# Kernel tuning notes

Measured on AMD Instinct MI355X. Metric: run time of the kernel, lower is better.

Reference implementation:

```python
import jax, jax.numpy as jnp
import numpy as np

B, S, D, H = 64, 512, 256, 512

def setup_inputs() -> dict:
    key = jax.random.key(0)
    ks = jax.random.split(key, 16)
    s_in = 1.0 / np.sqrt(D)
    s_h = 1.0 / np.sqrt(H)
    inp = {
        "inputs": jax.random.normal(ks[0], (B, S, D), jnp.float32),
        # input-side gate weights (stored [D,H], equiv to torch Linear weight.T)
        "Wf": jax.random.uniform(ks[1], (D, H), jnp.float32, -s_in, s_in),
        "Wi": jax.random.uniform(ks[2], (D, H), jnp.float32, -s_in, s_in),
        "Wo": jax.random.uniform(ks[3], (D, H), jnp.float32, -s_in, s_in),
        "Wc": jax.random.uniform(ks[4], (D, H), jnp.float32, -s_in, s_in),
        "bf": jax.random.uniform(ks[5], (H,), jnp.float32, -s_in, s_in),
        "bi": jax.random.uniform(ks[6], (H,), jnp.float32, -s_in, s_in),
        "bo": jax.random.uniform(ks[7], (H,), jnp.float32, -s_in, s_in),
        "bc": jax.random.uniform(ks[8], (H,), jnp.float32, -s_in, s_in),
        # recurrent weights (bias=False)
        "Uf": jax.random.uniform(ks[9], (H, H), jnp.float32, -s_h, s_h),
        "Ui": jax.random.uniform(ks[10], (H, H), jnp.float32, -s_h, s_h),
        "Uo": jax.random.uniform(ks[11], (H, H), jnp.float32, -s_h, s_h),
        "Uc": jax.random.uniform(ks[12], (H, H), jnp.float32, -s_h, s_h),
        # output head
        "Wfc": jax.random.uniform(ks[13], (H, 1), jnp.float32, -s_h, s_h),
        "bfc": jax.random.uniform(ks[14], (1,), jnp.float32, -s_h, s_h),
    }
    return inp


def reference(inputs, Wf, Wi, Wo, Wc, bf, bi, bo, bc, Uf, Ui, Uo, Uc, Wfc, bfc):
    # Precompute all input-side gate projections in one big GEMM: [B,S,4H]
    Wx = jnp.concatenate([Wf, Wi, Wo, Wc], axis=1)            # [D,4H]
    bx = jnp.concatenate([bf, bi, bo, bc], axis=0)            # [4H]
    gx = jnp.einsum('bsd,dg->bsg', inputs, Wx) + bx           # [B,S,4H]
    Uh = jnp.concatenate([Uf, Ui, Uo, Uc], axis=1)            # [H,4H]

    h0 = jnp.zeros((inputs.shape[0], Uf.shape[0]), inputs.dtype)
    c0 = jnp.zeros_like(h0)
    Hd = Uf.shape[0]

    def step(carry, gx_t):
        h, c = carry
        g = gx_t + h @ Uh                                     # [B,4H]
        f_t = jax.nn.sigmoid(g[:, 0 * Hd:1 * Hd])
        i_t = jax.nn.sigmoid(g[:, 1 * Hd:2 * Hd])
        o_t = jax.nn.sigmoid(g[:, 2 * Hd:3 * Hd])
        chat = jnp.tanh(g[:, 3 * Hd:4 * Hd])
        c = f_t * c + i_t * chat
        h = o_t * jnp.tanh(c)
        return (h, c), h

    (h_t, c_t), hs = jax.lax.scan(step, (h0, c0), jnp.swapaxes(gx, 0, 1))
    outputs = jnp.swapaxes(hs, 0, 1)                          # [B,S,H]
    predictions = jnp.einsum('bsh,ho->bso', outputs, Wfc) + bfc
    return predictions, h_t, c_t
```

## Files before the change

### kernel.cpp

```cpp
#include <hip/hip_runtime.h>
#include <hip/hip_bf16.h>

#define B_ 64
#define S_ 512
#define D_ 256
#define H_ 512

typedef __attribute__((ext_vector_type(8))) short bf16x8;
typedef __attribute__((ext_vector_type(4))) float f32x4;
typedef __attribute__((ext_vector_type(4))) unsigned int uint4v;
typedef unsigned short ushort_t;
typedef unsigned long long u64_t;

__device__ __forceinline__ ushort_t f2bf(float f) {
    __hip_bfloat16 h = __float2bfloat16(f);
    return *reinterpret_cast<ushort_t*>(&h);
}
__device__ __forceinline__ float sigmoid_f(float x) { return 1.f / (1.f + __expf(-x)); }
__device__ __forceinline__ float tanh_f(float x) { return 1.f - 2.f / (__expf(2.f * x) + 1.f); }

__device__ __forceinline__ void lds_barrier() {
    asm volatile("s_waitcnt lgkmcnt(0)\n\ts_barrier" ::: "memory");
}

__global__ __launch_bounds__(512) void lstm_rec(
    const float* __restrict__ X,
    const float* __restrict__ Wf, const float* __restrict__ Wi,
    const float* __restrict__ Wo, const float* __restrict__ Wc,
    const float* __restrict__ bfp, const float* __restrict__ bip,
    const float* __restrict__ bop, const float* __restrict__ bcp,
    const float* __restrict__ Uf, const float* __restrict__ Ui,
    const float* __restrict__ Uo, const float* __restrict__ Uc,
    const float* __restrict__ Wfc,
    float* __restrict__ pred, u64_t* __restrict__ hbuf,
    unsigned int* __restrict__ xcdtab,
    float* __restrict__ outH, float* __restrict__ outC)
{
    __shared__ ushort_t hS[16 * 520];
    __shared__ ushort_t xS[16 * 264];
    __shared__ float gact[4][16][68];
    __shared__ float predS[16][512];
    __shared__ int meta[2];

    const int tid  = threadIdx.x;
    const int w    = tid >> 6;
    const int lane = tid & 63;
    const int q    = lane >> 4;
    const int m    = lane & 15;
    const int gate = w >> 1;
    const int half = w & 1;

    if (w == 0) {
        unsigned int xcd;
        asm volatile("s_getreg_b32 %0, hwreg(HW_REG_XCC_ID)" : "=s"(xcd));
        xcd &= 15u;
        if (lane == 0)
            __hip_atomic_store(&xcdtab[blockIdx.x], xcd + 1u,
                               __ATOMIC_RELEASE, __HIP_MEMORY_SCOPE_AGENT);
        unsigned int entry;
        for (;;) {
            entry = __hip_atomic_load(&xcdtab[lane], __ATOMIC_ACQUIRE, __HIP_MEMORY_SCOPE_AGENT);
            if (__ballot(entry != 0u) == ~0ull) break;
            __builtin_amdgcn_s_sleep(1);
        }
        const unsigned int xcd_j = entry - 1u;
        const unsigned int key_j = (xcd_j << 8) | (unsigned int)lane;
        const unsigned int mykey = (xcd << 8) | (unsigned int)blockIdx.x;
        const int rank = __popcll(__ballot(key_j < mykey));
        const int c_lt = __popcll(__ballot(xcd_j < xcd));
        const int c_eq = __popcll(__ballot(xcd_j == xcd));
        const int gg   = rank >> 3;
        const bool uni = (c_lt <= gg * 8) && (gg * 8 + 8 <= c_lt + c_eq);
        if (lane == 0) { meta[0] = rank; meta[1] = uni ? 1 : 0; }
    }
    __syncthreads();
    const int  rank    = meta[0];
    const bool uniform = meta[1] != 0;
    if (rank >= 32) return;
    const int g = rank >> 3;
    const int s = rank & 7;

    const int ncol0 = s * 64 + half * 32 + m;
    const int ncol1 = ncol0 + 16;

    const float* Ug = (gate == 0) ? Uf : (gate == 1) ? Ui : (gate == 2) ? Uo : Uc;
    const float* Wg = (gate == 0) ? Wf : (gate == 1) ? Wi : (gate == 2) ? Wo : Wc;
    const float* bg = (gate == 0) ? bfp : (gate == 1) ? bip : (gate == 2) ? bop : bcp;

    const float bias0 = bg[ncol0];
    const float bias1 = bg[ncol1];

    bf16x8 UF[2][16];
    bf16x8 WF[2][8];
    #pragma unroll
    for (int tt = 0; tt < 2; ++tt) {
        const int nc = tt ? ncol1 : ncol0;
        #pragma unroll
        for (int ks = 0; ks < 16; ++ks) {
            bf16x8 v;
            #pragma unroll
            for (int j = 0; j < 8; ++j)
                v[j] = (short)f2bf(Ug[(ks * 32 + q * 8 + j) * H_ + nc]);
            UF[tt][ks] = v;
        }
        #pragma unroll
        for (int ks = 0; ks < 8; ++ks) {
            bf16x8 v;
            #pragma unroll
            for (int j = 0; j < 8; ++j)
                v[j] = (short)f2bf(Wg[(ks * 32 + q * 8 + j) * H_ + nc]);
            WF[tt][ks] = v;
        }
    }

    const int urow  = tid >> 5;
    const int upair = tid & 31;
    const float2 wfc2 = *(const float2*)&Wfc[s * 64 + 2 * upair];

    float cr0 = 0.f, cr1 = 0.f;

    #pragma unroll
    for (int i = 0; i < 16; ++i)
        predS[(tid * 16 + i) >> 9][(tid * 16 + i) & 511] = 0.f;
    {
        const float* xsrc = &X[((size_t)(g * 16 + urow) * S_ + 0) * D_ + upair * 8];
        float4 a = *(const float4*)xsrc;
        float4 b = *(const float4*)(xsrc + 4);
        bf16x8 v;
        v[0] = (short)f2bf(a.x); v[1] = (short)f2bf(a.y);
        v[2] = (short)f2bf(a.z); v[3] = (short)f2bf(a.w);
        v[4] = (short)f2bf(b.x); v[5] = (short)f2bf(b.y);
        v[6] = (short)f2bf(b.z); v[7] = (short)f2bf(b.w);
        *(bf16x8*)&xS[urow * 264 + upair * 8] = v;
    }

    float4 xr0, xr1;

    for (int t = 0; t < S_; ++t) {
        {
            const int row = tid >> 5;
            const int pr  = (tid & 31) * 8;
            u64_t* pe = hbuf + ((size_t)((t & 1) * B_ + g * 16 + row) * 256 + pr);
            const unsigned int tg = (unsigned int)t;
            uint4v ra, rb;
            bool got = false;
            if (uniform) {
                uint4v r0, r1, r2, r3;
                asm volatile(
                    "global_load_dwordx4 %0, %4, off sc0\n\t"
                    "global_load_dwordx4 %1, %5, off sc0\n\t"
                    "global_load_dwordx4 %2, %6, off sc0\n\t"
                    "global_load_dwordx4 %3, %7, off sc0\n\t"
                    "s_waitcnt vmcnt(0)"
                    : "=v"(r0), "=v"(r1), "=v"(r2), "=v"(r3)
                    : "v"(pe), "v"(pe + 2), "v"(pe + 4), "v"(pe + 6)
                    : "memory");
                bool ok = r0[1] == tg && r0[3] == tg && r1[1] == tg && r1[3] == tg
                       && r2[1] == tg && r2[3] == tg && r3[1] == tg && r3[3] == tg;
                if (__ballot(ok) == ~0ull) {
                    ra[0] = r0[0]; ra[1] = r0[2]; ra[2] = r1[0]; ra[3] = r1[2];
                    rb[0] = r2[0]; rb[1] = r2[2]; rb[2] = r3[0]; rb[3] = r3[2];
                    got = true;
                }
            }
            if (!got) {
                int rounds = 0;
                for (;;) {
                    u64_t e0 = __hip_atomic_load(pe + 0, __ATOMIC_RELAXED, __HIP_MEMORY_SCOPE_AGENT);
                    u64_t e1 = __hip_atomic_load(pe + 1, __ATOMIC_RELAXED, __HIP_MEMORY_SCOPE_AGENT);
                    u64_t e2 = __hip_atomic_load(pe + 2, __ATOMIC_RELAXED, __HIP_MEMORY_SCOPE_AGENT);
                    u64_t e3 = __hip_atomic_load(pe + 3, __ATOMIC_RELAXED, __HIP_MEMORY_SCOPE_AGENT);
                    u64_t e4 = __hip_atomic_load(pe + 4, __ATOMIC_RELAXED, __HIP_MEMORY_SCOPE_AGENT);
                    u64_t e5 = __hip_atomic_load(pe + 5, __ATOMIC_RELAXED, __HIP_MEMORY_SCOPE_AGENT);
                    u64_t e6 = __hip_atomic_load(pe + 6, __ATOMIC_RELAXED, __HIP_MEMORY_SCOPE_AGENT);
                    u64_t e7 = __hip_atomic_load(pe + 7, __ATOMIC_RELAXED, __HIP_MEMORY_SCOPE_AGENT);
                    bool ok = (unsigned int)(e0 >> 32) == tg && (unsigned int)(e1 >> 32) == tg
                           && (unsigned int)(e2 >> 32) == tg && (unsigned int)(e3 >> 32) == tg
                           && (unsigned int)(e4 >> 32) == tg && (unsigned int)(e5 >> 32) == tg
                           && (unsigned int)(e6 >> 32) == tg && (unsigned int)(e7 >> 32) == tg;
                    if (__ballot(ok) == ~0ull) {
                        ra[0] = (unsigned int)e0; ra[1] = (unsigned int)e1;
                        ra[2] = (unsigned int)e2; ra[3] = (unsigned int)e3;
                        rb[0] = (unsigned int)e4; rb[1] = (unsigned int)e5;
                        rb[2] = (unsigned int)e6; rb[3] = (unsigned int)e7;
                        break;
                    }
                    if (++rounds > 2) __builtin_amdgcn_s_sleep(1);
                }
            }
            if (t + 1 < S_) {
                const float* xsrc = &X[((size_t)(g * 16 + urow) * S_ + (t + 1)) * D_ + upair * 8];
                xr0 = *(const float4*)xsrc;
                xr1 = *(const float4*)(xsrc + 4);
            }
            *(uint4v*)&hS[row * 520 + pr * 2]     = ra;
            *(uint4v*)&hS[row * 520 + pr * 2 + 8] = rb;
        }
        lds_barrier();

        f32x4 accA0 = {bias0, bias0, bias0, bias0};
        f32x4 accA1 = {bias1, bias1, bias1, bias1};
        f32x4 accB0 = {0.f, 0.f, 0.f, 0.f};
        f32x4 accB1 = {0.f, 0.f, 0.f, 0.f};
        #pragma unroll
        for (int ks = 0; ks < 8; ++ks) {
            bf16x8 a = *(const bf16x8*)&xS[m * 264 + ks * 32 + q * 8];
            accA0 = __builtin_amdgcn_mfma_f32_16x16x32_bf16(a, WF[0][ks], accA0, 0, 0, 0);
            accA1 = __builtin_amdgcn_mfma_f32_16x16x32_bf16(a, WF[1][ks], accA1, 0, 0, 0);
        }
        #pragma unroll
        for (int ks = 0; ks < 16; ++ks) {
            bf16x8 a = *(const bf16x8*)&hS[m * 520 + ks * 32 + q * 8];
            accB0 = __builtin_amdgcn_mfma_f32_16x16x32_bf16(a, UF[0][ks], accB0, 0, 0, 0);
            accB1 = __builtin_amdgcn_mfma_f32_16x16x32_bf16(a, UF[1][ks], accB1, 0, 0, 0);
        }
        #pragma unroll
        for (int j = 0; j < 4; ++j) {
            float v0 = accA0[j] + accB0[j];
            float v1 = accA1[j] + accB1[j];
            v0 = (gate < 3) ? sigmoid_f(v0) : tanh_f(v0);
            v1 = (gate < 3) ? sigmoid_f(v1) : tanh_f(v1);
            gact[gate][q * 4 + j][half * 32 + m]      = v0;
            gact[gate][q * 4 + j][half * 32 + 16 + m] = v1;
        }
        lds_barrier();

        float2 f2v = *(const float2*)&gact[0][urow][2 * upair];
        float2 i2v = *(const float2*)&gact[1][urow][2 * upair];
        float2 o2v = *(const float2*)&gact[2][urow][2 * upair];
        float2 ch2 = *(const float2*)&gact[3][urow][2 * upair];
        cr0 = f2v.x * cr0 + i2v.x * ch2.x;
        cr1 = f2v.y * cr1 + i2v.y * ch2.y;
        float hv0 = o2v.x * tanh_f(cr0);
        float hv1 = o2v.y * tanh_f(cr1);

        if (t < S_ - 1) {
            unsigned int packed = (unsigned int)f2bf(hv0) | ((unsigned int)f2bf(hv1) << 16);
            u64_t ent = ((u64_t)(unsigned int)(t + 1) << 32) | (u64_t)packed;
            u64_t* hdst = hbuf + ((size_t)(((t + 1) & 1) * B_ + g * 16 + urow) * 256
                                  + s * 32 + upair);
            asm volatile("global_store_dwordx2 %0, %1, off sc0 sc1"
                         :: "v"(hdst), "v"(ent) : "memory");
            bf16x8 v;
            v[0] = (short)f2bf(xr0.x); v[1] = (short)f2bf(xr0.y);
            v[2] = (short)f2bf(xr0.z); v[3] = (short)f2bf(xr0.w);
            v[4] = (short)f2bf(xr1.x); v[5] = (short)f2bf(xr1.y);
            v[6] = (short)f2bf(xr1.z); v[7] = (short)f2bf(xr1.w);
            *(bf16x8*)&xS[urow * 264 + upair * 8] = v;
        } else {
            *(float2*)&outH[(g * 16 + urow) * H_ + s * 64 + 2 * upair] = make_float2(hv0, hv1);
            *(float2*)&outC[(g * 16 + urow) * H_ + s * 64 + 2 * upair] = make_float2(cr0, cr1);
        }

        float pv = hv0 * wfc2.x + hv1 * wfc2.y;
        pv += __shfl_xor(pv, 16);
        pv += __shfl_xor(pv, 8);
        pv += __shfl_xor(pv, 4);
        pv += __shfl_xor(pv, 2);
        pv += __shfl_xor(pv, 1);
        if (upair == 0) predS[urow][t] = pv;
    }

    lds_barrier();
    #pragma unroll
    for (int i = 0; i < 16; ++i) {
        const int idx = tid * 16 + i;
        const int row = idx >> 9;
        const int tt  = idx & 511;
        atomicAdd(&pred[(g * 16 + row) * S_ + tt], predS[row][tt]);
    }
}

__global__ void pred_fin(const float* __restrict__ pred,
                         const float* __restrict__ bfc,
                         float* __restrict__ out)
{
    int i = blockIdx.x * blockDim.x + threadIdx.x;
    if (i < B_ * S_) out[i] = pred[i] + bfc[0];
}

extern "C" void kernel_launch(void* const* d_in, const int* in_sizes, int n_in,
                              void* d_out, int out_size, void* d_ws, size_t ws_size,
                              hipStream_t stream) {
    const float* X   = (const float*)d_in[0];
    const float* Wf  = (const float*)d_in[1];
    const float* Wi  = (const float*)d_in[2];
    const float* Wo  = (const float*)d_in[3];
    const float* Wc  = (const float*)d_in[4];
    const float* bfp = (const float*)d_in[5];
    const float* bip = (const float*)d_in[6];
    const float* bop = (const float*)d_in[7];
    const float* bcp = (const float*)d_in[8];
    const float* Uf  = (const float*)d_in[9];
    const float* Ui  = (const float*)d_in[10];
    const float* Uo  = (const float*)d_in[11];
    const float* Uc  = (const float*)d_in[12];
    const float* Wfc = (const float*)d_in[13];
    const float* bfc = (const float*)d_in[14];

    float*        pred   = (float*)d_ws;
    u64_t*        hbuf   = (u64_t*)((char*)d_ws + 131072);
    unsigned int* xcdtab = (unsigned int*)((char*)d_ws + 393216);

    hipMemsetAsync(d_ws, 0, 393216 + 256, stream);

    float* out = (float*)d_out;
    lstm_rec<<<64, 512, 0, stream>>>(X, Wf, Wi, Wo, Wc, bfp, bip, bop, bcp,
                                     Uf, Ui, Uo, Uc, Wfc,
                                     pred, hbuf, xcdtab,
                                     out + 32768, out + 65536);
    pred_fin<<<128, 256, 0, stream>>>(pred, bfc, out);
}
```

Before: 2.286 ms.

## Split waves into consumer and producer roles for cross-block h exchange

Threads are divided so the first 256 poll and load the shared hidden-state buffer and the x prefetch, each handling twice as much, while the other 256 publish h. The publishing threads stage the block's h in LDS, then write it as wider dwordx4 stores after an extra barrier. The aim is to shorten the critical path of the per-step global handoff and reduce the number of store instructions. It adds an LDS barrier every step and puts more load work on half the threads. The always-sleep backoff in the polling fallback may add latency.

```diff
diff --git a/kernel.cpp b/kernel.cpp
--- a/kernel.cpp
+++ b/kernel.cpp
@@ -39,6 +39,7 @@
     __shared__ ushort_t hS[16 * 520];
     __shared__ ushort_t xS[16 * 264];
     __shared__ float gact[4][16][68];
+    __shared__ unsigned int hOutS[16][32];
     __shared__ float predS[16][512];
     __shared__ int meta[2];
 
@@ -80,6 +81,8 @@
     const int g = rank >> 3;
     const int s = rank & 7;
 
+    const bool cons = (tid < 256);
+
     const int ncol0 = s * 64 + half * 32 + m;
     const int ncol1 = ncol0 + 16;
 
@@ -119,82 +122,110 @@
 
     float cr0 = 0.f, cr1 = 0.f;
 
+    const int crow   = tid >> 4;
+    const int cchunk = tid & 15;
+    u64_t* peA = hbuf + ((size_t)(0 * B_ + g * 16 + crow) * 256 + cchunk * 16);
+    u64_t* peB = hbuf + ((size_t)(1 * B_ + g * 16 + crow) * 256 + cchunk * 16);
+    const int xs0 = tid * 2, xs1 = tid * 2 + 1;
+    const int xrow0 = xs0 >> 5, xup0 = xs0 & 31;
+    const int xrow1 = xs1 >> 5, xup1 = xs1 & 31;
+
     #pragma unroll
     for (int i = 0; i < 16; ++i)
         predS[(tid * 16 + i) >> 9][(tid * 16 + i) & 511] = 0.f;
-    {
-        const float* xsrc = &X[((size_t)(g * 16 + urow) * S_ + 0) * D_ + upair * 8];
-        float4 a = *(const float4*)xsrc;
-        float4 b = *(const float4*)(xsrc + 4);
+    if (cons) {
+        const float* xa = &X[((size_t)(g * 16 + xrow0) * S_ + 0) * D_ + xup0 * 8];
+        const float* xb = &X[((size_t)(g * 16 + xrow1) * S_ + 0) * D_ + xup1 * 8];
+        float4 a0 = *(const float4*)xa, a1 = *(const float4*)(xa + 4);
+        float4 b0 = *(const float4*)xb, b1 = *(const float4*)(xb + 4);
         bf16x8 v;
-        v[0] = (short)f2bf(a.x); v[1] = (short)f2bf(a.y);
-        v[2] = (short)f2bf(a.z); v[3] = (short)f2bf(a.w);
-        v[4] = (short)f2bf(b.x); v[5] = (short)f2bf(b.y);
-        v[6] = (short)f2bf(b.z); v[7] = (short)f2bf(b.w);
-        *(bf16x8*)&xS[urow * 264 + upair * 8] = v;
-    }
-
-    float4 xr0, xr1;
+        v[0] = (short)f2bf(a0.x); v[1] = (short)f2bf(a0.y);
+        v[2] = (short)f2bf(a0.z); v[3] = (short)f2bf(a0.w);
+        v[4] = (short)f2bf(a1.x); v[5] = (short)f2bf(a1.y);
+        v[6] = (short)f2bf(a1.z); v[7] = (short)f2bf(a1.w);
+        *(bf16x8*)&xS[xrow0 * 264 + xup0 * 8] = v;
+        v[0] = (short)f2bf(b0.x); v[1] = (short)f2bf(b0.y);
+        v[2] = (short)f2bf(b0.z); v[3] = (short)f2bf(b0.w);
+        v[4] = (short)f2bf(b1.x); v[5] = (short)f2bf(b1.y);
+        v[6] = (short)f2bf(b1.z); v[7] = (short)f2bf(b1.w);
+        *(bf16x8*)&xS[xrow1 * 264 + xup1 * 8] = v;
+    }
+
+    float4 xr00, xr01, xr10, xr11;
 
     for (int t = 0; t < S_; ++t) {
-        {
-            const int row = tid >> 5;
-            const int pr  = (tid & 31) * 8;
-            u64_t* pe = hbuf + ((size_t)((t & 1) * B_ + g * 16 + row) * 256 + pr);
+        if (cons) {
+            u64_t* pe = (t & 1) ? peB : peA;
             const unsigned int tg = (unsigned int)t;
-            uint4v ra, rb;
+            uint4v ra0, ra1, ra2, ra3;
             bool got = false;
             if (uniform) {
-                uint4v r0, r1, r2, r3;
+                uint4v r0, r1, r2, r3, r4, r5, r6, r7;
+                asm volatile(
+                    "global_load_dwordx4 %0, %4, off sc0\n\t"
+                    "global_load_dwordx4 %1, %5, off sc0\n\t"
+                    "global_load_dwordx4 %2, %6, off sc0\n\t"
+                    "global_load_dwordx4 %3, %7, off sc0"
+                    : "=v"(r0), "=v"(r1), "=v"(r2), "=v"(r3)
+                    : "v"(pe), "v"(pe + 2), "v"(pe + 4), "v"(pe + 6)
+                    : "memory");
                 asm volatile(
                     "global_load_dwordx4 %0, %4, off sc0\n\t"
                     "global_load_dwordx4 %1, %5, off sc0\n\t"
                     "global_load_dwordx4 %2, %6, off sc0\n\t"
                     "global_load_dwordx4 %3, %7, off sc0\n\t"
                     "s_waitcnt vmcnt(0)"
-                    : "=v"(r0), "=v"(r1), "=v"(r2), "=v"(r3)
-                    : "v"(pe), "v"(pe + 2), "v"(pe + 4), "v"(pe + 6)
+                    : "=v"(r4), "=v"(r5), "=v"(r6), "=v"(r7)
+                    : "v"(pe + 8), "v"(pe + 10), "v"(pe + 12), "v"(pe + 14)
                     : "memory");
                 bool ok = r0[1] == tg && r0[3] == tg && r1[1] == tg && r1[3] == tg
-                       && r2[1] == tg && r2[3] == tg && r3[1] == tg && r3[3] == tg;
+                       && r2[1] == tg && r2[3] == tg && r3[1] == tg && r3[3] == tg
+                       && r4[1] == tg && r4[3] == tg && r5[1] == tg && r5[3] == tg
+                       && r6[1] == tg && r6[3] == tg && r7[1] == tg && r7[3] == tg;
                 if (__ballot(ok) == ~0ull) {
-                    ra[0] = r0[0]; ra[1] = r0[2]; ra[2] = r1[0]; ra[3] = r1[2];
-                    rb[0] = r2[0]; rb[1] = r2[2]; rb[2] = r3[0]; rb[3] = r3[2];
+                    ra0[0] = r0[0]; ra0[1] = r0[2]; ra0[2] = r1[0]; ra0[3] = r1[2];
+                    ra1[0] = r2[0]; ra1[1] = r2[2]; ra1[2] = r3[0]; ra1[3] = r3[2];
+                    ra2[0] = r4[0]; ra2[1] = r4[2]; ra2[2] = r5[0]; ra2[3] = r5[2];
+                    ra3[0] = r6[0]; ra3[1] = r6[2]; ra3[2] = r7[0]; ra3[3] = r7[2];
                     got = true;
                 }
             }
             if (!got) {
-                int rounds = 0;
                 for (;;) {
-                    u64_t e0 = __hip_atomic_load(pe + 0, __ATOMIC_RELAXED, __HIP_MEMORY_SCOPE_AGENT);
-                    u64_t e1 = __hip_atomic_load(pe + 1, __ATOMIC_RELAXED, __HIP_MEMORY_SCOPE_AGENT);
-                    u64_t e2 = __hip_atomic_load(pe + 2, __ATOMIC_RELAXED, __HIP_MEMORY_SCOPE_AGENT);
-                    u64_t e3 = __hip_atomic_load(pe + 3, __ATOMIC_RELAXED, __HIP_MEMORY_SCOPE_AGENT);
-                    u64_t e4 = __hip_atomic_load(pe + 4, __ATOMIC_RELAXED, __HIP_MEMORY_SCOPE_AGENT);
-                    u64_t e5 = __hip_atomic_load(pe + 5, __ATOMIC_RELAXED, __HIP_MEMORY_SCOPE_AGENT);
-                    u64_t e6 = __hip_atomic_load(pe + 6, __ATOMIC_RELAXED, __HIP_MEMORY_SCOPE_AGENT);
-                    u64_t e7 = __hip_atomic_load(pe + 7, __ATOMIC_RELAXED, __HIP_MEMORY_SCOPE_AGENT);
-                    bool ok = (unsigned int)(e0 >> 32) == tg && (unsigned int)(e1 >> 32) == tg
-                           && (unsigned int)(e2 >> 32) == tg && (unsigned int)(e3 >> 32) == tg
-                           && (unsigned int)(e4 >> 32) == tg && (unsigned int)(e5 >> 32) == tg
-                           && (unsigned int)(e6 >> 32) == tg && (unsigned int)(e7 >> 32) == tg;
+                    u64_t ev[16];
+                    #pragma unroll
+                    for (int e = 0; e < 16; ++e)
+                        ev[e] = __hip_atomic_load(pe + e, __ATOMIC_RELAXED,
+                                                  __HIP_MEMORY_SCOPE_AGENT);
+                    bool ok = true;
+                    #pragma unroll
+                    for (int e = 0; e < 16; ++e)
+                        ok = ok && ((unsigned int)(ev[e] >> 32) == tg);
                     if (__ballot(ok) == ~0ull) {
-                        ra[0] = (unsigned int)e0; ra[1] = (unsigned int)e1;
-                        ra[2] = (unsigned int)e2; ra[3] = (unsigned int)e3;
-                        rb[0] = (unsigned int)e4; rb[1] = (unsigned int)e5;
-                        rb[2] = (unsigned int)e6; rb[3] = (unsigned int)e7;
+                        ra0[0] = (unsigned int)ev[0];  ra0[1] = (unsigned int)ev[1];
+                        ra0[2] = (unsigned int)ev[2];  ra0[3] = (unsigned int)ev[3];
+                        ra1[0] = (unsigned int)ev[4];  ra1[1] = (unsigned int)ev[5];
+                        ra1[2] = (unsigned int)ev[6];  ra1[3] = (unsigned int)ev[7];
+                        ra2[0] = (unsigned int)ev[8];  ra2[1] = (unsigned int)ev[9];
+                        ra2[2] = (unsigned int)ev[10]; ra2[3] = (unsigned int)ev[11];
+                        ra3[0] = (unsigned int)ev[12]; ra3[1] = (unsigned int)ev[13];
+                        ra3[2] = (unsigned int)ev[14]; ra3[3] = (unsigned int)ev[15];
                         break;
                     }
-                    if (++rounds > 2) __builtin_amdgcn_s_sleep(1);
+                    __builtin_amdgcn_s_sleep(1);
                 }
             }
             if (t + 1 < S_) {
-                const float* xsrc = &X[((size_t)(g * 16 + urow) * S_ + (t + 1)) * D_ + upair * 8];
-                xr0 = *(const float4*)xsrc;
-                xr1 = *(const float4*)(xsrc + 4);
+                const float* xa = &X[((size_t)(g * 16 + xrow0) * S_ + (t + 1)) * D_ + xup0 * 8];
+                const float* xb = &X[((size_t)(g * 16 + xrow1) * S_ + (t + 1)) * D_ + xup1 * 8];
+                xr00 = *(const float4*)xa; xr01 = *(const float4*)(xa + 4);
+                xr10 = *(const float4*)xb; xr11 = *(const float4*)(xb + 4);
             }
-            *(uint4v*)&hS[row * 520 + pr * 2]     = ra;
-            *(uint4v*)&hS[row * 520 + pr * 2 + 8] = rb;
+            ushort_t* hb = &hS[crow * 520 + cchunk * 32];
+            *(uint4v*)(hb)      = ra0;
+            *(uint4v*)(hb + 8)  = ra1;
+            *(uint4v*)(hb + 16) = ra2;
+            *(uint4v*)(hb + 24) = ra3;
         }
         lds_barrier();
 
@@ -234,20 +265,23 @@
         float hv0 = o2v.x * tanh_f(cr0);
         float hv1 = o2v.y * tanh_f(cr1);
 
-        if (t < S_ - 1) {
-            unsigned int packed = (unsigned int)f2bf(hv0) | ((unsigned int)f2bf(hv1) << 16);
-            u64_t ent = ((u64_t)(unsigned int)(t + 1) << 32) | (u64_t)packed;
-            u64_t* hdst = hbuf + ((size_t)(((t + 1) & 1) * B_ + g * 16 + urow) * 256
-                                  + s * 32 + upair);
-            asm volatile("global_store_dwordx2 %0, %1, off sc0 sc1"
-                         :: "v"(hdst), "v"(ent) : "memory");
+        hOutS[urow][upair] = (unsigned int)f2bf(hv0) | ((unsigned int)f2bf(hv1) << 16);
+
+        if (cons && t + 1 < S_) {
             bf16x8 v;
-            v[0] = (short)f2bf(xr0.x); v[1] = (short)f2bf(xr0.y);
-            v[2] = (short)f2bf(xr0.z); v[3] = (short)f2bf(xr0.w);
-            v[4] = (short)f2bf(xr1.x); v[5] = (short)f2bf(xr1.y);
-            v[6] = (short)f2bf(xr1.z); v[7] = (short)f2bf(xr1.w);
-            *(bf16x8*)&xS[urow * 264 + upair * 8] = v;
-        } else {
+            v[0] = (short)f2bf(xr00.x); v[1] = (short)f2bf(xr00.y);
+            v[2] = (short)f2bf(xr00.z); v[3] = (short)f2bf(xr00.w);
+            v[4] = (short)f2bf(xr01.x); v[5] = (short)f2bf(xr01.y);
+            v[6] = (short)f2bf(xr01.z); v[7] = (short)f2bf(xr01.w);
+            *(bf16x8*)&xS[xrow0 * 264 + xup0 * 8] = v;
+            v[0] = (short)f2bf(xr10.x); v[1] = (short)f2bf(xr10.y);
+            v[2] = (short)f2bf(xr10.z); v[3] = (short)f2bf(xr10.w);
+            v[4] = (short)f2bf(xr11.x); v[5] = (short)f2bf(xr11.y);
+            v[6] = (short)f2bf(xr11.z); v[7] = (short)f2bf(xr11.w);
+            *(bf16x8*)&xS[xrow1 * 264 + xup1 * 8] = v;
+        }
+
+        if (t == S_ - 1) {
             *(float2*)&outH[(g * 16 + urow) * H_ + s * 64 + 2 * upair] = make_float2(hv0, hv1);
             *(float2*)&outC[(g * 16 + urow) * H_ + s * 64 + 2 * upair] = make_float2(cr0, cr1);
         }
@@ -259,6 +293,24 @@
         pv += __shfl_xor(pv, 2);
         pv += __shfl_xor(pv, 1);
         if (upair == 0) predS[urow][t] = pv;
+
+        lds_barrier();
+
+        if (!cons && t + 1 < S_) {
+            asm volatile("s_waitcnt vmcnt(40)" ::: "memory");
+            const unsigned int tv = (unsigned int)(t + 1);
+            const int eidx = (tid - 256) * 2;
+            const int erow = eidx >> 5;
+            const int eup  = eidx & 31;
+            unsigned int d0 = hOutS[erow][eup];
+            unsigned int d1 = hOutS[erow][eup + 1];
+            uint4v st;
+            st[0] = d0; st[1] = tv; st[2] = d1; st[3] = tv;
+            u64_t* hdst = hbuf + ((size_t)(((t + 1) & 1) * B_ + g * 16 + erow) * 256
+                                  + s * 32 + eup);
+            asm volatile("global_store_dwordx4 %0, %1, off sc0 sc1"
+                         :: "v"(hdst), "v"(st) : "memory");
+        }
     }
 
     lds_barrier();
@@ -302,7 +354,7 @@
     u64_t*        hbuf   = (u64_t*)((char*)d_ws + 131072);
     unsigned int* xcdtab = (unsigned int*)((char*)d_ws + 393216);
 
-    hipMemsetAsync(d_ws, 0, 393216 + 256, stream);
+    hipMemsetAsync(d_ws, 0, 393472, stream);
 
     float* out = (float*)d_out;
     lstm_rec<<<64, 512, 0, stream>>>(X, Wf, Wi, Wo, Wc, bfp, bip, bop, bcp,
```

Measured after the change: 4.357 ms. 90.6% more time.
